# Performance work log

Hardware: AMD Instinct MI355X
Metric: run time of the kernel (lower is better)

The kernel has to match this reference:

```python
import jax, jax.numpy as jnp
import numpy as np

N = 50000
E = 1_600_000
H = 128          # hidden_dim
HEADS = 4
PH = H // 2      # platform embedding dim = 64
LRELU_SLOPE = 0.2
BN_EPS = 1e-5


def _lin_init(key, fan_in, fan_out):
    return jax.random.normal(key, (fan_in, fan_out), jnp.float32) / np.sqrt(fan_in)


def setup_inputs() -> dict:
    key = jax.random.key(0)
    ks = jax.random.split(key, 32)
    inp = {}
    inp["x"] = jax.random.normal(ks[0], (N, 10), jnp.float32)
    inp["edge_index"] = jax.random.randint(ks[1], (2, E), 0, N, jnp.int32)
    inp["platform_x"] = jax.random.normal(ks[2], (1, 4), jnp.float32)
    # node encoder
    inp["node_W"] = _lin_init(ks[3], 10, H); inp["node_b"] = jnp.zeros((H,))
    # platform encoder
    inp["plat_W"] = _lin_init(ks[4], 4, PH); inp["plat_b"] = jnp.zeros((PH,))
    # GAT layers: W [in, heads*out], att vectors [1, heads, out], bias [heads*out]
    inp["g1_W"] = _lin_init(ks[5], H, H)
    inp["g1_asrc"] = jax.random.normal(ks[6], (1, HEADS, H // HEADS)) * 0.1
    inp["g1_adst"] = jax.random.normal(ks[7], (1, HEADS, H // HEADS)) * 0.1
    inp["g1_b"] = jnp.zeros((H,))
    inp["g2_W"] = _lin_init(ks[8], H, H)
    inp["g2_asrc"] = jax.random.normal(ks[9], (1, HEADS, H // HEADS)) * 0.1
    inp["g2_adst"] = jax.random.normal(ks[10], (1, HEADS, H // HEADS)) * 0.1
    inp["g2_b"] = jnp.zeros((H,))
    inp["g3_W"] = _lin_init(ks[11], H, H)
    inp["g3_asrc"] = jax.random.normal(ks[12], (1, 1, H)) * 0.1
    inp["g3_adst"] = jax.random.normal(ks[13], (1, 1, H)) * 0.1
    inp["g3_b"] = jnp.zeros((H,))
    # BatchNorm (eval mode: running_mean=0, running_var=1)
    for i, k in zip((1, 2, 3), (ks[14], ks[15], ks[16])):
        inp[f"bn{i}_g"] = jnp.ones((H,)) + 0.1 * jax.random.normal(k, (H,))
        inp[f"bn{i}_b"] = jnp.zeros((H,))
    # classifier: 192 -> 128 -> 64 -> 3
    inp["c1_W"] = _lin_init(ks[17], H + PH, H); inp["c1_b"] = jnp.zeros((H,))
    inp["c2_W"] = _lin_init(ks[18], H, PH);     inp["c2_b"] = jnp.zeros((PH,))
    inp["c3_W"] = _lin_init(ks[19], PH, 3);     inp["c3_b"] = jnp.zeros((3,))
    return inp


def gat_conv(x, src, dst, W, a_src, a_dst, b, heads, out_dim, n):
    # PyG GATConv (eval, self-loops already appended): gather -> edge score ->
    # segment softmax over destination -> scatter-add.
    h = (x @ W).reshape(n, heads, out_dim)              # [N, heads, out]
    al_s = jnp.sum(h * a_src, axis=-1)                  # [N, heads]
    al_d = jnp.sum(h * a_dst, axis=-1)                  # [N, heads]
    e = jax.nn.leaky_relu(al_s[src] + al_d[dst], LRELU_SLOPE)  # [E, heads]
    m = jax.ops.segment_max(e, dst, num_segments=n)
    m = jnp.where(jnp.isfinite(m), m, 0.0)
    ex = jnp.exp(e - m[dst])
    s = jax.ops.segment_sum(ex, dst, num_segments=n)
    alpha = ex / (s[dst] + 1e-16)                       # [E, heads]
    out = jax.ops.segment_sum(alpha[:, :, None] * h[src], dst, num_segments=n)
    return out.reshape(n, heads * out_dim) + b


def bn_eval(x, g, b):
    # running_mean=0, running_var=1 -> x / sqrt(1+eps) * g + b
    return x * (g / np.sqrt(1.0 + BN_EPS)) + b


def reference(x, edge_index, platform_x, node_W, node_b, plat_W, plat_b,
              g1_W, g1_asrc, g1_adst, g1_b, g2_W, g2_asrc, g2_adst, g2_b,
              g3_W, g3_asrc, g3_adst, g3_b, bn1_g, bn1_b, bn2_g, bn2_b,
              bn3_g, bn3_b, c1_W, c1_b, c2_W, c2_b, c3_W, c3_b):
    n = x.shape[0]
    loops = jnp.arange(n, dtype=edge_index.dtype)
    src = jnp.concatenate([edge_index[0], loops])
    dst = jnp.concatenate([edge_index[1], loops])

    h = jax.nn.relu(x @ node_W + node_b)
    h = gat_conv(h, src, dst, g1_W, g1_asrc, g1_adst, g1_b, HEADS, H // HEADS, n)
    h = jax.nn.relu(bn_eval(h, bn1_g, bn1_b))
    h = gat_conv(h, src, dst, g2_W, g2_asrc, g2_adst, g2_b, HEADS, H // HEADS, n)
    h = jax.nn.relu(bn_eval(h, bn2_g, bn2_b))
    h = gat_conv(h, src, dst, g3_W, g3_asrc, g3_adst, g3_b, 1, H, n)
    h = jax.nn.relu(bn_eval(h, bn3_g, bn3_b))

    p = jax.nn.relu(platform_x @ plat_W + plat_b)       # [1, PH]
    p = jnp.broadcast_to(p[0:1], (n, PH))
    h = jnp.concatenate([h, p], axis=1)                 # [N, H+PH]

    h = jax.nn.relu(h @ c1_W + c1_b)
    h = jax.nn.relu(h @ c2_W + c2_b)
    return h @ c3_W + c3_b                              # [N, 3]
```

## Files before the change

kernel.cpp:

```cpp
#include <hip/hip_runtime.h>
#include <hip/hip_bf16.h>
#include <hip/hip_fp16.h>

#define LRELU 0.2f
#define BN_INVS 0.99999500003749968f

__global__ __launch_bounds__(256) void k_initdeg(int* deg, int n) {
    int i = blockIdx.x * 256 + threadIdx.x;
    if (i < n) deg[i] = 1;
}

__global__ __launch_bounds__(256) void k_count(const int* __restrict__ ei, int* deg, int E) {
    int e = blockIdx.x * 256 + threadIdx.x;
    if (e < E) atomicAdd(&deg[ei[E + e]], 1);
}

__global__ __launch_bounds__(1024) void k_scan1(const int* __restrict__ deg, int* row_ptr,
                                                int* bsum, int n) {
    __shared__ int sm[1024];
    int t = threadIdx.x, g = blockIdx.x * 1024 + t;
    sm[t] = (g < n) ? deg[g] : 0;
    __syncthreads();
    for (int off = 1; off < 1024; off <<= 1) {
        int x = (t >= off) ? sm[t - off] : 0;
        __syncthreads();
        sm[t] += x;
        __syncthreads();
    }
    if (g < n) row_ptr[g + 1] = sm[t];
    if (t == 1023) bsum[blockIdx.x] = sm[t];
}

__global__ void k_scan2(const int* bsum, int* boff, int nb) {
    if (threadIdx.x == 0 && blockIdx.x == 0) {
        int s = 0;
        for (int i = 0; i < nb; ++i) { boff[i] = s; s += bsum[i]; }
    }
}

__global__ __launch_bounds__(1024) void k_scan3(int* row_ptr, const int* boff, int n) {
    int g = blockIdx.x * 1024 + threadIdx.x;
    if (g < n) row_ptr[g + 1] += boff[blockIdx.x];
    if (g == 0) row_ptr[0] = 0;
}

__global__ __launch_bounds__(256) void k_cursor(const int* __restrict__ rp, int* cur, int n) {
    int i = blockIdx.x * 256 + threadIdx.x;
    if (i < n) cur[i] = rp[i];
}

__global__ __launch_bounds__(256) void k_scatter(const int* __restrict__ ei, int* cur, int* col,
                                                 int E, int n) {
    int g = blockIdx.x & 7;
    int W = (n + 7) >> 3;
    int lo = g * W;
    int hi = min(n, lo + W);
    int nb = gridDim.x >> 3;
    int bi = blockIdx.x >> 3;
    int stride = nb * 256;
    for (int t = bi * 256 + threadIdx.x; t < E; t += stride) {
        int d = ei[E + t];
        if (d >= lo && d < hi) {
            int p = atomicAdd(&cur[d], 1);
            col[p] = ei[t];
        }
    }
    for (int v = lo + bi * 256 + threadIdx.x; v < hi; v += stride) {
        int p = atomicAdd(&cur[v], 1);
        col[p] = v;
    }
}

__global__ __launch_bounds__(256) void k_node_enc(const float* __restrict__ x,
                                                  const float* __restrict__ W,
                                                  const float* __restrict__ b,
                                                  float* __restrict__ h, int n) {
    __shared__ float Ws[1280];
    __shared__ float bs[128];
    for (int i = threadIdx.x; i < 1280; i += 256) Ws[i] = W[i];
    if (threadIdx.x < 128) bs[threadIdx.x] = b[threadIdx.x];
    __syncthreads();
    int idx = blockIdx.x * 256 + threadIdx.x;
    if (idx >= n * 32) return;
    int v = idx >> 5, q = idx & 31;
    float xr[10];
#pragma unroll
    for (int i = 0; i < 10; ++i) xr[i] = x[v * 10 + i];
    float o[4];
#pragma unroll
    for (int j = 0; j < 4; ++j) {
        int c = q * 4 + j;
        float s = bs[c];
#pragma unroll
        for (int i = 0; i < 10; ++i) s += xr[i] * Ws[i * 128 + c];
        o[j] = fmaxf(s, 0.f);
    }
    *(float4*)(h + (size_t)v * 128 + q * 4) = make_float4(o[0], o[1], o[2], o[3]);
}

template <int M, bool ADD_BIAS, bool RELU, bool HALF_OUT = false>
__global__ __launch_bounds__(256) void k_gemm128(const float* __restrict__ A,
                                                 const float* __restrict__ B,
                                                 const float* __restrict__ bias,
                                                 float* __restrict__ C, int n) {
    constexpr int NG = M / 64;
    __shared__ float AsT[32][133];
    __shared__ float Bs[32][M];
    int tid = threadIdx.x;
    int row0 = blockIdx.x * 128;
    int ct = tid & 15, rt = tid >> 4;
    float4 acc[8][NG];
#pragma unroll
    for (int i = 0; i < 8; ++i)
#pragma unroll
        for (int g = 0; g < NG; ++g) acc[i][g] = make_float4(0.f, 0.f, 0.f, 0.f);

    for (int kc = 0; kc < 128; kc += 32) {
#pragma unroll
        for (int i = 0; i < 4; ++i) {
            int f = tid + i * 256;
            int r = f >> 3;
            int kq = (f & 7) * 4;
            float4 v = make_float4(0.f, 0.f, 0.f, 0.f);
            int gr = row0 + r;
            if (gr < n) v = *(const float4*)(A + (size_t)gr * 128 + kc + kq);
            AsT[kq + 0][r] = v.x;
            AsT[kq + 1][r] = v.y;
            AsT[kq + 2][r] = v.z;
            AsT[kq + 3][r] = v.w;
        }
#pragma unroll
        for (int i = 0; i < M / 32; ++i) {
            int f = tid + i * 256;
            int r = f / (M / 4), c4 = (f % (M / 4)) * 4;
            *(float4*)(&Bs[r][c4]) = *(const float4*)(B + (size_t)(kc + r) * M + c4);
        }
        __syncthreads();
#pragma unroll
        for (int k = 0; k < 32; ++k) {
            float4 a0 = *(const float4*)(&AsT[k][rt * 8]);
            float4 a1 = *(const float4*)(&AsT[k][rt * 8 + 4]);
            float av[8] = {a0.x, a0.y, a0.z, a0.w, a1.x, a1.y, a1.z, a1.w};
#pragma unroll
            for (int g = 0; g < NG; ++g) {
                float4 bv = *(const float4*)(&Bs[k][g * 64 + ct * 4]);
#pragma unroll
                for (int i = 0; i < 8; ++i) {
                    acc[i][g].x += av[i] * bv.x;
                    acc[i][g].y += av[i] * bv.y;
                    acc[i][g].z += av[i] * bv.z;
                    acc[i][g].w += av[i] * bv.w;
                }
            }
        }
        __syncthreads();
    }
    float4 bb[NG];
    if (ADD_BIAS) {
#pragma unroll
        for (int g = 0; g < NG; ++g) bb[g] = *(const float4*)(bias + g * 64 + ct * 4);
    }
#pragma unroll
    for (int i = 0; i < 8; ++i) {
        int gr = row0 + rt * 8 + i;
        if (gr < n) {
#pragma unroll
            for (int g = 0; g < NG; ++g) {
                float4 v = acc[i][g];
                if (ADD_BIAS) {
                    v.x += bb[g].x; v.y += bb[g].y; v.z += bb[g].z; v.w += bb[g].w;
                }
                if (RELU) {
                    v.x = fmaxf(v.x, 0.f); v.y = fmaxf(v.y, 0.f);
                    v.z = fmaxf(v.z, 0.f); v.w = fmaxf(v.w, 0.f);
                }
                if (HALF_OUT) {
                    __half hb[4];
                    hb[0] = __float2half(v.x);
                    hb[1] = __float2half(v.y);
                    hb[2] = __float2half(v.z);
                    hb[3] = __float2half(v.w);
                    __half* C16 = reinterpret_cast<__half*>(C);
                    *(ushort4*)(C16 + (size_t)gr * M + g * 64 + ct * 4) = *(ushort4*)hb;
                } else {
                    *(float4*)(C + (size_t)gr * M + g * 64 + ct * 4) = v;
                }
            }
        }
    }
}

template <int HEADS>
__global__ __launch_bounds__(256) void k_al(const __half* __restrict__ hw,
                                            const float* __restrict__ asrc,
                                            const float* __restrict__ adst,
                                            float* __restrict__ al_s, float* __restrict__ al_d,
                                            int n) {
    int wid = (blockIdx.x * 256 + threadIdx.x) >> 6;
    int l = threadIdx.x & 63;
    if (wid >= n) return;
    unsigned raw = *(const unsigned*)(hw + (size_t)wid * 128 + 2 * l);
    __half2 hp = *reinterpret_cast<__half2*>(&raw);
    float2 hv = __half22float2(hp);
    int c0 = 2 * l;
    if (HEADS == 4) {
        int h = l >> 4, dd = c0 & 31;
        float s = hv.x * asrc[h * 32 + dd] + hv.y * asrc[h * 32 + dd + 1];
        float d = hv.x * adst[h * 32 + dd] + hv.y * adst[h * 32 + dd + 1];
#pragma unroll
        for (int off = 1; off < 16; off <<= 1) {
            s += __shfl_xor(s, off);
            d += __shfl_xor(d, off);
        }
        if ((l & 15) == 0) {
            al_s[wid * 4 + h] = s;
            al_d[wid * 4 + h] = d;
        }
    } else {
        float s = hv.x * asrc[c0] + hv.y * asrc[c0 + 1];
        float d = hv.x * adst[c0] + hv.y * adst[c0 + 1];
#pragma unroll
        for (int off = 1; off < 64; off <<= 1) {
            s += __shfl_xor(s, off);
            d += __shfl_xor(d, off);
        }
        if (l == 0) {
            al_s[wid] = s;
            al_d[wid] = d;
        }
    }
}

template <int HEADS>
__global__ __launch_bounds__(256) void k_softagg(const int* __restrict__ rp,
                                                 const int* __restrict__ col,
                                                 const float* __restrict__ al_s,
                                                 const float* __restrict__ al_d,
                                                 const __half* __restrict__ hw,
                                                 const float* __restrict__ gb,
                                                 const float* __restrict__ bng,
                                                 const float* __restrict__ bnb,
                                                 float* __restrict__ hout, int n) {
    constexpr int CAP = 128;
    __shared__ int ss[4][CAP];
    __shared__ __align__(16) float se[4][CAP * HEADS];
    int v = (blockIdx.x * 256 + threadIdx.x) >> 6;
    int l = threadIdx.x & 63;
    int w = threadIdx.x >> 6;
    if (v >= n) return;
    int start = rp[v], end = rp[v + 1];
    int deg = end - start;

    float ad[HEADS], m[HEADS], s[HEADS], inv[HEADS];
#pragma unroll
    for (int h = 0; h < HEADS; ++h) {
        ad[h] = al_d[v * HEADS + h];
        m[h] = -1e30f;
        s[h] = 0.f;
    }

    if (deg <= CAP) {
        for (int p = start + l; p < end; p += 64) {
            int src = col[p];
            float eh[HEADS];
            if (HEADS == 4) {
                float4 t4 = *(const float4*)(al_s + (size_t)src * 4);
                eh[0] = t4.x; eh[1] = t4.y; eh[2] = t4.z; eh[3] = t4.w;
            } else {
                eh[0] = al_s[src];
            }
#pragma unroll
            for (int h = 0; h < HEADS; ++h) {
                float e = eh[h] + ad[h];
                eh[h] = (e >= 0.f) ? e : LRELU * e;
                m[h] = fmaxf(m[h], eh[h]);
            }
            int idx = p - start;
            ss[w][idx] = src;
            if (HEADS == 4)
                *(float4*)(&se[w][idx * 4]) = make_float4(eh[0], eh[1], eh[2], eh[3]);
            else
                se[w][idx] = eh[0];
        }
#pragma unroll
        for (int off = 1; off < 64; off <<= 1)
#pragma unroll
            for (int h = 0; h < HEADS; ++h) m[h] = fmaxf(m[h], __shfl_xor(m[h], off));

        for (int idx = l; idx < deg; idx += 64) {
            if (HEADS == 4) {
                float4 e4 = *(float4*)(&se[w][idx * 4]);
                e4.x = __expf(e4.x - m[0]);
                e4.y = __expf(e4.y - m[1]);
                e4.z = __expf(e4.z - m[2]);
                e4.w = __expf(e4.w - m[3]);
                *(float4*)(&se[w][idx * 4]) = e4;
                s[0] += e4.x; s[1] += e4.y; s[2] += e4.z; s[3] += e4.w;
            } else {
                float a = __expf(se[w][idx] - m[0]);
                se[w][idx] = a;
                s[0] += a;
            }
        }
#pragma unroll
        for (int off = 1; off < 64; off <<= 1)
#pragma unroll
            for (int h = 0; h < HEADS; ++h) s[h] += __shfl_xor(s[h], off);
#pragma unroll
        for (int h = 0; h < HEADS; ++h) inv[h] = 1.f / (s[h] + 1e-16f);

        int qe = l >> 4;
        int li = l & 15;
        int c8 = li * 8;
        int hd = (HEADS == 4) ? (li >> 2) : 0;
        float invh = inv[hd];
        float acc[8] = {0.f, 0.f, 0.f, 0.f, 0.f, 0.f, 0.f, 0.f};
        for (int p = start + qe; p < end; p += 4) {
            int idx = p - start;
            int s0 = ss[w][idx];
            float a0 = (HEADS == 4) ? se[w][idx * 4 + hd] : se[w][idx];
            uint4 r = *(const uint4*)(hw + (size_t)s0 * 128 + c8);
            float2 f0 = __half22float2(*reinterpret_cast<__half2*>(&r.x));
            float2 f1 = __half22float2(*reinterpret_cast<__half2*>(&r.y));
            float2 f2 = __half22float2(*reinterpret_cast<__half2*>(&r.z));
            float2 f3 = __half22float2(*reinterpret_cast<__half2*>(&r.w));
            acc[0] += a0 * f0.x; acc[1] += a0 * f0.y;
            acc[2] += a0 * f1.x; acc[3] += a0 * f1.y;
            acc[4] += a0 * f2.x; acc[5] += a0 * f2.y;
            acc[6] += a0 * f3.x; acc[7] += a0 * f3.y;
        }
#pragma unroll
        for (int j = 0; j < 8; ++j) {
            acc[j] += __shfl_xor(acc[j], 16);
            acc[j] += __shfl_xor(acc[j], 32);
        }
        if (l < 16) {
#pragma unroll
            for (int half = 0; half < 2; ++half) {
                int c4 = c8 + half * 4;
                float4 g4 = *(const float4*)(gb + c4);
                float4 bg = *(const float4*)(bng + c4);
                float4 bbv = *(const float4*)(bnb + c4);
                float4 o;
                o.x = fmaxf((acc[half * 4 + 0] * invh + g4.x) * (bg.x * BN_INVS) + bbv.x, 0.f);
                o.y = fmaxf((acc[half * 4 + 1] * invh + g4.y) * (bg.y * BN_INVS) + bbv.y, 0.f);
                o.z = fmaxf((acc[half * 4 + 2] * invh + g4.z) * (bg.z * BN_INVS) + bbv.z, 0.f);
                o.w = fmaxf((acc[half * 4 + 3] * invh + g4.w) * (bg.w * BN_INVS) + bbv.w, 0.f);
                *(float4*)(hout + (size_t)v * 128 + c4) = o;
            }
        }
        return;
    }

    for (int p = start + l; p < end; p += 64) {
        int src = col[p];
        float eh[HEADS];
        if (HEADS == 4) {
            float4 t4 = *(const float4*)(al_s + (size_t)src * 4);
            eh[0] = t4.x; eh[1] = t4.y; eh[2] = t4.z; eh[3] = t4.w;
        } else {
            eh[0] = al_s[src];
        }
#pragma unroll
        for (int h = 0; h < HEADS; ++h) {
            float e = eh[h] + ad[h];
            e = (e >= 0.f) ? e : LRELU * e;
            float nm = fmaxf(m[h], e);
            s[h] = s[h] * __expf(m[h] - nm) + __expf(e - nm);
            m[h] = nm;
        }
    }
#pragma unroll
    for (int off = 1; off < 64; off <<= 1) {
#pragma unroll
        for (int h = 0; h < HEADS; ++h) {
            float om = __shfl_xor(m[h], off), os = __shfl_xor(s[h], off);
            float nm = fmaxf(m[h], om);
            s[h] = s[h] * __expf(m[h] - nm) + os * __expf(om - nm);
            m[h] = nm;
        }
    }
#pragma unroll
    for (int h = 0; h < HEADS; ++h) inv[h] = 1.f / (s[h] + 1e-16f);

    int ew = l >> 5;
    int li = l & 31;
    int c4 = 4 * li;
    int hd = (HEADS == 4) ? (li >> 3) : 0;
    float mh = m[hd], invh = inv[hd], adh = ad[hd];
    float4 acc = make_float4(0.f, 0.f, 0.f, 0.f);
    for (int p = start + ew; p < end; p += 2) {
        int s0 = col[p];
        float t = al_s[(size_t)s0 * HEADS + hd] + adh;
        float e0 = (t >= 0.f) ? t : LRELU * t;
        float a0 = __expf(e0 - mh);
        uint2 r0 = *(const uint2*)(hw + (size_t)s0 * 128 + c4);
        float2 f00 = __half22float2(*reinterpret_cast<__half2*>(&r0.x));
        float2 f01 = __half22float2(*reinterpret_cast<__half2*>(&r0.y));
        acc.x += a0 * f00.x;
        acc.y += a0 * f00.y;
        acc.z += a0 * f01.x;
        acc.w += a0 * f01.y;
    }
    acc.x += __shfl_xor(acc.x, 32);
    acc.y += __shfl_xor(acc.y, 32);
    acc.z += __shfl_xor(acc.z, 32);
    acc.w += __shfl_xor(acc.w, 32);
    if (l < 32) {
        float4 g4 = *(const float4*)(gb + c4);
        float4 bg = *(const float4*)(bng + c4);
        float4 bbv = *(const float4*)(bnb + c4);
        float4 o;
        o.x = fmaxf((acc.x * invh + g4.x) * (bg.x * BN_INVS) + bbv.x, 0.f);
        o.y = fmaxf((acc.y * invh + g4.y) * (bg.y * BN_INVS) + bbv.y, 0.f);
        o.z = fmaxf((acc.z * invh + g4.z) * (bg.z * BN_INVS) + bbv.z, 0.f);
        o.w = fmaxf((acc.w * invh + g4.w) * (bg.w * BN_INVS) + bbv.w, 0.f);
        *(float4*)(hout + (size_t)v * 128 + c4) = o;
    }
}

__global__ void k_pconst(const float* __restrict__ px, const float* __restrict__ pW,
                         const float* __restrict__ pb, const float* __restrict__ c1W,
                         const float* __restrict__ c1b, float* __restrict__ cvec) {
    __shared__ float p[64];
    int t = threadIdx.x;
    if (t < 64) {
        float s = pb[t];
#pragma unroll
        for (int i = 0; i < 4; ++i) s += px[i] * pW[i * 64 + t];
        p[t] = fmaxf(s, 0.f);
    }
    __syncthreads();
    if (t < 128) {
        float s = c1b[t];
#pragma unroll
        for (int j = 0; j < 64; ++j) s += p[j] * c1W[(128 + j) * 128 + t];
        cvec[t] = s;
    }
}

__global__ __launch_bounds__(256) void k_c3(const float* __restrict__ h5,
                                            const float* __restrict__ W,
                                            const float* __restrict__ b, float* __restrict__ out,
                                            int n) {
    __shared__ float Ws[192];
    __shared__ float bs[3];
    if (threadIdx.x < 192) Ws[threadIdx.x] = W[threadIdx.x];
    if (threadIdx.x < 3) bs[threadIdx.x] = b[threadIdx.x];
    __syncthreads();
    int v = blockIdx.x * 256 + threadIdx.x;
    if (v >= n) return;
    float a0 = bs[0], a1 = bs[1], a2 = bs[2];
#pragma unroll
    for (int k4 = 0; k4 < 16; ++k4) {
        float4 xv = *(const float4*)(h5 + (size_t)v * 64 + k4 * 4);
        int k = k4 * 4;
        a0 += xv.x * Ws[k * 3 + 0] + xv.y * Ws[k * 3 + 3] + xv.z * Ws[k * 3 + 6] + xv.w * Ws[k * 3 + 9];
        a1 += xv.x * Ws[k * 3 + 1] + xv.y * Ws[k * 3 + 4] + xv.z * Ws[k * 3 + 7] + xv.w * Ws[k * 3 + 10];
        a2 += xv.x * Ws[k * 3 + 2] + xv.y * Ws[k * 3 + 5] + xv.z * Ws[k * 3 + 8] + xv.w * Ws[k * 3 + 11];
    }
    out[v * 3 + 0] = a0;
    out[v * 3 + 1] = a1;
    out[v * 3 + 2] = a2;
}

extern "C" void kernel_launch(void* const* d_in, const int* in_sizes, int n_in,
                              void* d_out, int out_size, void* d_ws, size_t ws_size,
                              hipStream_t stream) {
    const float* x      = (const float*)d_in[0];
    const int*   ei     = (const int*)d_in[1];
    const float* px     = (const float*)d_in[2];
    const float* node_W = (const float*)d_in[3];
    const float* node_b = (const float*)d_in[4];
    const float* plat_W = (const float*)d_in[5];
    const float* plat_b = (const float*)d_in[6];
    const float* g1_W = (const float*)d_in[7];
    const float* g1_as = (const float*)d_in[8];
    const float* g1_ad = (const float*)d_in[9];
    const float* g1_b = (const float*)d_in[10];
    const float* g2_W = (const float*)d_in[11];
    const float* g2_as = (const float*)d_in[12];
    const float* g2_ad = (const float*)d_in[13];
    const float* g2_b = (const float*)d_in[14];
    const float* g3_W = (const float*)d_in[15];
    const float* g3_as = (const float*)d_in[16];
    const float* g3_ad = (const float*)d_in[17];
    const float* g3_b = (const float*)d_in[18];
    const float* bn1_g = (const float*)d_in[19];
    const float* bn1_b = (const float*)d_in[20];
    const float* bn2_g = (const float*)d_in[21];
    const float* bn2_b = (const float*)d_in[22];
    const float* bn3_g = (const float*)d_in[23];
    const float* bn3_b = (const float*)d_in[24];
    const float* c1_W = (const float*)d_in[25];
    const float* c1_b = (const float*)d_in[26];
    const float* c2_W = (const float*)d_in[27];
    const float* c2_b = (const float*)d_in[28];
    const float* c3_W = (const float*)d_in[29];
    const float* c3_b = (const float*)d_in[30];

    const int N = in_sizes[0] / 10;
    const int E = in_sizes[1] / 2;
    const int ET = E + N;

    char* w = (char*)d_ws;
    auto alloc = [&](size_t bytes) {
        void* p = (void*)w;
        w += (bytes + 255) & ~(size_t)255;
        return p;
    };
    int*   col     = (int*)alloc((size_t)ET * 4);
    int*   deg     = (int*)alloc((size_t)N * 4);
    int*   row_ptr = (int*)alloc((size_t)(N + 1) * 4);
    int*   bsum    = (int*)alloc(256 * 4);
    int*   boff    = (int*)alloc(256 * 4);
    float* al_s    = (float*)alloc((size_t)N * 4 * 4);
    float* al_d    = (float*)alloc((size_t)N * 4 * 4);
    float* bufA    = (float*)alloc((size_t)N * 128 * 4);
    float* bufB    = (float*)alloc((size_t)N * 128 * 4);
    float* cvec    = (float*)alloc(128 * 4);
    float* out     = (float*)d_out;
    __half* h16    = (__half*)bufB;

    const int NB = (N + 1023) / 1024;

    k_initdeg<<<(N + 255) / 256, 256, 0, stream>>>(deg, N);
    k_count<<<(E + 255) / 256, 256, 0, stream>>>(ei, deg, E);
    k_scan1<<<NB, 1024, 0, stream>>>(deg, row_ptr, bsum, N);
    k_scan2<<<1, 64, 0, stream>>>(bsum, boff, NB);
    k_scan3<<<NB, 1024, 0, stream>>>(row_ptr, boff, N);
    k_cursor<<<(N + 255) / 256, 256, 0, stream>>>(row_ptr, deg, N);
    k_scatter<<<3328, 256, 0, stream>>>(ei, deg, col, E, N);

    k_node_enc<<<(N * 32 + 255) / 256, 256, 0, stream>>>(x, node_W, node_b, bufA, N);

    const int gGemm = (N + 127) / 128;
    const int gWave = (N * 64 + 255) / 256;

    k_gemm128<128, false, false, true><<<gGemm, 256, 0, stream>>>(bufA, g1_W, nullptr, (float*)h16, N);
    k_al<4><<<gWave, 256, 0, stream>>>(h16, g1_as, g1_ad, al_s, al_d, N);
    k_softagg<4><<<gWave, 256, 0, stream>>>(row_ptr, col, al_s, al_d, h16, g1_b, bn1_g, bn1_b, bufA, N);

    k_gemm128<128, false, false, true><<<gGemm, 256, 0, stream>>>(bufA, g2_W, nullptr, (float*)h16, N);
    k_al<4><<<gWave, 256, 0, stream>>>(h16, g2_as, g2_ad, al_s, al_d, N);
    k_softagg<4><<<gWave, 256, 0, stream>>>(row_ptr, col, al_s, al_d, h16, g2_b, bn2_g, bn2_b, bufA, N);

    k_gemm128<128, false, false, true><<<gGemm, 256, 0, stream>>>(bufA, g3_W, nullptr, (float*)h16, N);
    k_al<1><<<gWave, 256, 0, stream>>>(h16, g3_as, g3_ad, al_s, al_d, N);
    k_softagg<1><<<gWave, 256, 0, stream>>>(row_ptr, col, al_s, al_d, h16, g3_b, bn3_g, bn3_b, bufA, N);

    k_pconst<<<1, 128, 0, stream>>>(px, plat_W, plat_b, c1_W, c1_b, cvec);

    k_gemm128<128, true, true><<<gGemm, 256, 0, stream>>>(bufA, c1_W, cvec, bufB, N);
    k_gemm128<64, true, true><<<gGemm, 256, 0, stream>>>(bufB, c2_W, c2_b, bufA, N);
    k_c3<<<(N + 255) / 256, 256, 0, stream>>>(bufA, c3_W, c3_b, out, N);
}
```

Baseline: 720.6 us.

## Retile node GEMMs to 64x64 blocks and use nontemporal loads for edge index

The GEMM kernel is rewritten from 128-row blocks covering all output columns to 64x64 output tiles on a 2D grid, with each thread computing a 4x4 patch. This gives more blocks and lower register pressure, which is meant to improve occupancy and balance across compute units, at the cost of less register reuse per loaded value and more redundant loads of A across column tiles. Edge-index reads in the count and scatter kernels now use nontemporal loads so the streamed indices do not pollute the cache. In the scatter kernel the source index is now loaded only for edges whose destination falls in the block's range.

```diff
diff --git a/kernel.cpp b/kernel.cpp
--- a/kernel.cpp
+++ b/kernel.cpp
@@ -12,7 +12,7 @@
 
 __global__ __launch_bounds__(256) void k_count(const int* __restrict__ ei, int* deg, int E) {
     int e = blockIdx.x * 256 + threadIdx.x;
-    if (e < E) atomicAdd(&deg[ei[E + e]], 1);
+    if (e < E) atomicAdd(&deg[__builtin_nontemporal_load(&ei[E + e]) ? (ei[E + e]) : ei[E + e]], 1);
 }
 
 __global__ __launch_bounds__(1024) void k_scan1(const int* __restrict__ deg, int* row_ptr,
@@ -59,10 +59,11 @@
     int bi = blockIdx.x >> 3;
     int stride = nb * 256;
     for (int t = bi * 256 + threadIdx.x; t < E; t += stride) {
-        int d = ei[E + t];
+        int d = __builtin_nontemporal_load(ei + E + t);
         if (d >= lo && d < hi) {
+            int s = __builtin_nontemporal_load(ei + t);
             int p = atomicAdd(&cur[d], 1);
-            col[p] = ei[t];
+            col[p] = s;
         }
     }
     for (int v = lo + bi * 256 + threadIdx.x; v < hi; v += stride) {
@@ -99,25 +100,23 @@
 }
 
 template <int M, bool ADD_BIAS, bool RELU, bool HALF_OUT = false>
-__global__ __launch_bounds__(256) void k_gemm128(const float* __restrict__ A,
-                                                 const float* __restrict__ B,
-                                                 const float* __restrict__ bias,
-                                                 float* __restrict__ C, int n) {
-    constexpr int NG = M / 64;
-    __shared__ float AsT[32][133];
-    __shared__ float Bs[32][M];
+__global__ __launch_bounds__(256) void k_gemm64(const float* __restrict__ A,
+                                                const float* __restrict__ B,
+                                                const float* __restrict__ bias,
+                                                float* __restrict__ C, int n) {
+    __shared__ float AsT[32][68];
+    __shared__ float Bs[32][68];
     int tid = threadIdx.x;
-    int row0 = blockIdx.x * 128;
+    int row0 = blockIdx.x * 64;
+    int col0 = blockIdx.y * 64;
     int ct = tid & 15, rt = tid >> 4;
-    float4 acc[8][NG];
-#pragma unroll
-    for (int i = 0; i < 8; ++i)
-#pragma unroll
-        for (int g = 0; g < NG; ++g) acc[i][g] = make_float4(0.f, 0.f, 0.f, 0.f);
+    float4 acc[4];
+#pragma unroll
+    for (int i = 0; i < 4; ++i) acc[i] = make_float4(0.f, 0.f, 0.f, 0.f);
 
     for (int kc = 0; kc < 128; kc += 32) {
 #pragma unroll
-        for (int i = 0; i < 4; ++i) {
+        for (int i = 0; i < 2; ++i) {
             int f = tid + i * 256;
             int r = f >> 3;
             int kq = (f & 7) * 4;
@@ -130,61 +129,48 @@
             AsT[kq + 3][r] = v.w;
         }
 #pragma unroll
-        for (int i = 0; i < M / 32; ++i) {
+        for (int i = 0; i < 2; ++i) {
             int f = tid + i * 256;
-            int r = f / (M / 4), c4 = (f % (M / 4)) * 4;
-            *(float4*)(&Bs[r][c4]) = *(const float4*)(B + (size_t)(kc + r) * M + c4);
+            int r = f >> 4;
+            int c4 = (f & 15) * 4;
+            *(float4*)(&Bs[r][c4]) = *(const float4*)(B + (size_t)(kc + r) * M + col0 + c4);
         }
         __syncthreads();
 #pragma unroll
         for (int k = 0; k < 32; ++k) {
-            float4 a0 = *(const float4*)(&AsT[k][rt * 8]);
-            float4 a1 = *(const float4*)(&AsT[k][rt * 8 + 4]);
-            float av[8] = {a0.x, a0.y, a0.z, a0.w, a1.x, a1.y, a1.z, a1.w};
-#pragma unroll
-            for (int g = 0; g < NG; ++g) {
-                float4 bv = *(const float4*)(&Bs[k][g * 64 + ct * 4]);
-#pragma unroll
-                for (int i = 0; i < 8; ++i) {
-                    acc[i][g].x += av[i] * bv.x;
-                    acc[i][g].y += av[i] * bv.y;
-                    acc[i][g].z += av[i] * bv.z;
-                    acc[i][g].w += av[i] * bv.w;
-                }
-            }
+            float4 av = *(const float4*)(&AsT[k][rt * 4]);
+            float4 bv = *(const float4*)(&Bs[k][ct * 4]);
+            acc[0].x += av.x * bv.x; acc[0].y += av.x * bv.y; acc[0].z += av.x * bv.z; acc[0].w += av.x * bv.w;
+            acc[1].x += av.y * bv.x; acc[1].y += av.y * bv.y; acc[1].z += av.y * bv.z; acc[1].w += av.y * bv.w;
+            acc[2].x += av.z * bv.x; acc[2].y += av.z * bv.y; acc[2].z += av.z * bv.z; acc[2].w += av.z * bv.w;
+            acc[3].x += av.w * bv.x; acc[3].y += av.w * bv.y; acc[3].z += av.w * bv.z; acc[3].w += av.w * bv.w;
         }
         __syncthreads();
     }
-    float4 bb[NG];
-    if (ADD_BIAS) {
-#pragma unroll
-        for (int g = 0; g < NG; ++g) bb[g] = *(const float4*)(bias + g * 64 + ct * 4);
-    }
-#pragma unroll
-    for (int i = 0; i < 8; ++i) {
-        int gr = row0 + rt * 8 + i;
+    float4 bb = make_float4(0.f, 0.f, 0.f, 0.f);
+    if (ADD_BIAS) bb = *(const float4*)(bias + col0 + ct * 4);
+#pragma unroll
+    for (int i = 0; i < 4; ++i) {
+        int gr = row0 + rt * 4 + i;
         if (gr < n) {
-#pragma unroll
-            for (int g = 0; g < NG; ++g) {
-                float4 v = acc[i][g];
-                if (ADD_BIAS) {
-                    v.x += bb[g].x; v.y += bb[g].y; v.z += bb[g].z; v.w += bb[g].w;
-                }
-                if (RELU) {
-                    v.x = fmaxf(v.x, 0.f); v.y = fmaxf(v.y, 0.f);
-                    v.z = fmaxf(v.z, 0.f); v.w = fmaxf(v.w, 0.f);
-                }
-                if (HALF_OUT) {
-                    __half hb[4];
-                    hb[0] = __float2half(v.x);
-                    hb[1] = __float2half(v.y);
-                    hb[2] = __float2half(v.z);
-                    hb[3] = __float2half(v.w);
-                    __half* C16 = reinterpret_cast<__half*>(C);
-                    *(ushort4*)(C16 + (size_t)gr * M + g * 64 + ct * 4) = *(ushort4*)hb;
-                } else {
-                    *(float4*)(C + (size_t)gr * M + g * 64 + ct * 4) = v;
-                }
+            float4 v = acc[i];
+            if (ADD_BIAS) {
+                v.x += bb.x; v.y += bb.y; v.z += bb.z; v.w += bb.w;
+            }
+            if (RELU) {
+                v.x = fmaxf(v.x, 0.f); v.y = fmaxf(v.y, 0.f);
+                v.z = fmaxf(v.z, 0.f); v.w = fmaxf(v.w, 0.f);
+            }
+            if (HALF_OUT) {
+                __half hb[4];
+                hb[0] = __float2half(v.x);
+                hb[1] = __float2half(v.y);
+                hb[2] = __float2half(v.z);
+                hb[3] = __float2half(v.w);
+                __half* C16 = reinterpret_cast<__half*>(C);
+                *(ushort4*)(C16 + (size_t)gr * M + col0 + ct * 4) = *(ushort4*)hb;
+            } else {
+                *(float4*)(C + (size_t)gr * M + col0 + ct * 4) = v;
             }
         }
     }
@@ -534,24 +520,25 @@
 
     k_node_enc<<<(N * 32 + 255) / 256, 256, 0, stream>>>(x, node_W, node_b, bufA, N);
 
-    const int gGemm = (N + 127) / 128;
+    const dim3 g128((N + 63) / 64, 2);
+    const dim3 g64((N + 63) / 64, 1);
     const int gWave = (N * 64 + 255) / 256;
 
-    k_gemm128<128, false, false, true><<<gGemm, 256, 0, stream>>>(bufA, g1_W, nullptr, (float*)h16, N);
+    k_gemm64<128, false, false, true><<<g128, 256, 0, stream>>>(bufA, g1_W, nullptr, (float*)h16, N);
     k_al<4><<<gWave, 256, 0, stream>>>(h16, g1_as, g1_ad, al_s, al_d, N);
     k_softagg<4><<<gWave, 256, 0, stream>>>(row_ptr, col, al_s, al_d, h16, g1_b, bn1_g, bn1_b, bufA, N);
 
-    k_gemm128<128, false, false, true><<<gGemm, 256, 0, stream>>>(bufA, g2_W, nullptr, (float*)h16, N);
+    k_gemm64<128, false, false, true><<<g128, 256, 0, stream>>>(bufA, g2_W, nullptr, (float*)h16, N);
     k_al<4><<<gWave, 256, 0, stream>>>(h16, g2_as, g2_ad, al_s, al_d, N);
     k_softagg<4><<<gWave, 256, 0, stream>>>(row_ptr, col, al_s, al_d, h16, g2_b, bn2_g, bn2_b, bufA, N);
 
-    k_gemm128<128, false, false, true><<<gGemm, 256, 0, stream>>>(bufA, g3_W, nullptr, (float*)h16, N);
+    k_gemm64<128, false, false, true><<<g128, 256, 0, stream>>>(bufA, g3_W, nullptr, (float*)h16, N);
     k_al<1><<<gWave, 256, 0, stream>>>(h16, g3_as, g3_ad, al_s, al_d, N);
     k_softagg<1><<<gWave, 256, 0, stream>>>(row_ptr, col, al_s, al_d, h16, g3_b, bn3_g, bn3_b, bufA, N);
 
     k_pconst<<<1, 128, 0, stream>>>(px, plat_W, plat_b, c1_W, c1_b, cvec);
 
-    k_gemm128<128, true, true><<<gGemm, 256, 0, stream>>>(bufA, c1_W, cvec, bufB, N);
-    k_gemm128<64, true, true><<<gGemm, 256, 0, stream>>>(bufB, c2_W, c2_b, bufA, N);
+    k_gemm64<128, true, true><<<g128, 256, 0, stream>>>(bufA, c1_W, cvec, bufB, N);
+    k_gemm64<64, true, true><<<g64, 256, 0, stream>>>(bufB, c2_W, c2_b, bufA, N);
     k_c3<<<(N + 255) / 256, 256, 0, stream>>>(bufA, c3_W, c3_b, out, N);
 }
```

Result: faster. 628.7 us (-12.8%).
